# Kernel tuning notes

Hardware: AMD Instinct MI355X
Metric: run time of the kernel (lower is better)

The kernel has to match this reference:

```python
import jax, jax.numpy as jnp
import numpy as np

D_MODEL, D_STATE, D_CONV, EXPAND, L = 512, 16, 4, 2, 2048
D_INNER = EXPAND * D_MODEL


def _dwconv_causal(x, w, b):
    # x: (L, D), w: (D, K), b: (D,). torch Conv1d(groups=D, padding=K-1)[..., :L]
    K = w.shape[1]
    xp = jnp.pad(x, ((K - 1, 0), (0, 0)))
    windows = jnp.stack([xp[k:k + x.shape[0]] for k in range(K)], axis=-1)  # (L, D, K)
    return jnp.einsum('ldk,dk->ld', windows, w) + b


def _ssm_dir(x, inW, inb, cw, cb, xpW, xpb, dtW, dtb, outW, outb, A_log, Dp):
    xz = x @ inW + inb                      # (L, 2*Di)
    x_ssm, z = xz[:, :D_INNER], xz[:, D_INNER:]
    x_ssm = _dwconv_causal(x_ssm, cw, cb)   # (L, Di)
    sp = jax.nn.silu(x_ssm) @ xpW + xpb     # (L, Di + 2*S)
    delta = sp[:, :D_INNER]
    B = sp[:, D_INNER:D_INNER + D_STATE]
    C = sp[:, D_INNER + D_STATE:]
    dt = jax.nn.softplus(delta @ dtW + dtb)  # (L, Di)
    A = -jnp.exp(A_log)                      # (Di, S)
    dA = jnp.exp(dt[:, :, None] * A[None])                      # (L, Di, S)
    dBu = dt[:, :, None] * B[:, None, :] * x_ssm[:, :, None]    # (L, Di, S)

    def step(h, inp):
        a, bu = inp
        h = a * h + bu
        return h, h

    h0 = jnp.zeros((D_INNER, D_STATE), x.dtype)
    _, hs = jax.lax.scan(step, h0, (dA, dBu))   # (L, Di, S)
    y = jnp.einsum('lds,ls->ld', hs, C) + Dp * x_ssm
    return (y * jax.nn.silu(z)) @ outW + outb


def _make_params(key):
    ks = jax.random.split(key, 32)
    i = iter(range(32))
    def w(shape, scale=0.02):
        return (jax.random.normal(ks[next(i)], shape, jnp.float32) * scale)
    p = {}
    for pre in ('fwd_', 'bwd_'):
        p[pre + 'in_W'] = w((D_MODEL, 2 * D_INNER))
        p[pre + 'in_b'] = w((2 * D_INNER,))
        p[pre + 'conv_w'] = w((D_INNER, D_CONV), 0.1)
        p[pre + 'conv_b'] = w((D_INNER,))
        p[pre + 'xp_W'] = w((D_INNER, D_INNER + 2 * D_STATE))
        p[pre + 'xp_b'] = w((D_INNER + 2 * D_STATE,))
        p[pre + 'dt_W'] = w((D_INNER, D_INNER))
        p[pre + 'dt_b'] = w((D_INNER,))
        p[pre + 'out_W'] = w((D_INNER, D_MODEL))
        p[pre + 'out_b'] = w((D_MODEL,))
    p['A_log'] = jax.random.normal(ks[next(i)], (D_INNER, D_STATE), jnp.float32) * 0.5
    p['D_param'] = jnp.ones((D_INNER,), jnp.float32)
    p['fusion_W'] = w((2 * D_MODEL, D_MODEL))
    p['fusion_b'] = w((D_MODEL,))
    return p


def setup_inputs() -> dict:
    key = jax.random.key(0)
    kx, kp = jax.random.split(key)
    inp = {'x': jax.random.normal(kx, (L, D_MODEL), jnp.float32)}
    inp.update(_make_params(kp))
    return inp


def reference(x,
              fwd_in_W, fwd_in_b, fwd_conv_w, fwd_conv_b, fwd_xp_W, fwd_xp_b,
              fwd_dt_W, fwd_dt_b, fwd_out_W, fwd_out_b,
              bwd_in_W, bwd_in_b, bwd_conv_w, bwd_conv_b, bwd_xp_W, bwd_xp_b,
              bwd_dt_W, bwd_dt_b, bwd_out_W, bwd_out_b,
              A_log, D_param, fusion_W, fusion_b):
    out_fwd = _ssm_dir(x, fwd_in_W, fwd_in_b, fwd_conv_w, fwd_conv_b,
                       fwd_xp_W, fwd_xp_b, fwd_dt_W, fwd_dt_b,
                       fwd_out_W, fwd_out_b, A_log, D_param)
    out_bwd = _ssm_dir(x[::-1], bwd_in_W, bwd_in_b, bwd_conv_w, bwd_conv_b,
                       bwd_xp_W, bwd_xp_b, bwd_dt_W, bwd_dt_b,
                       bwd_out_W, bwd_out_b, A_log, D_param)[::-1]
    return jnp.concatenate([out_fwd, out_bwd], axis=-1) @ fusion_W + fusion_b
```

## Files before the change

kernel.cpp:

```cpp
#include <hip/hip_runtime.h>
#include <cmath>

#define L_SEQ 2048
#define DM 512
#define DI 1024
#define DS 16
#define NSP 1056
#define NC 64
#define CL 32

typedef unsigned short ushortT;
typedef unsigned int u32;
typedef __attribute__((ext_vector_type(8))) short short8;
typedef __attribute__((ext_vector_type(4))) float float4_t;
typedef __attribute__((address_space(1))) u32 gu32;
typedef __attribute__((address_space(3))) u32 lu32;

__device__ __forceinline__ float sigm(float x) { return 1.0f / (1.0f + __expf(-x)); }

__device__ __forceinline__ ushortT f2bf(float f) {
    unsigned u = __float_as_uint(f);
    unsigned r = u + 0x7FFFu + ((u >> 16) & 1u);
    return (ushortT)(r >> 16);
}
__device__ __forceinline__ float b2f(ushortT u) {
    return __uint_as_float(((u32)u) << 16);
}

__device__ __forceinline__ void gl2lds16(const ushortT* g, ushortT* l) {
    __builtin_amdgcn_global_load_lds((gu32*)g, (lu32*)l, 16, 0, 0);
}

struct WC {
    const float* src[11];
    ushortT* dst[11];
    int ss[11], soff[11], ds_[11], tN[11], mode[11];
    int off[12];
};

__global__ __launch_bounds__(256) void prep_all(
    WC wc, int nW,
    const float* __restrict__ x, ushortT* __restrict__ xb,
    const float* __restrict__ xpb0, const float* __restrict__ xpb1,
    const float* __restrict__ dtW0, const float* __restrict__ dtW1,
    const float* __restrict__ dtb0, const float* __restrict__ dtb1,
    const float* __restrict__ outb0, const float* __restrict__ outb1,
    const float* __restrict__ fuW, const float* __restrict__ fub,
    float* __restrict__ BFdt0, float* __restrict__ BFdt1, float* __restrict__ BFof)
{
    __shared__ ushortT t[32][33];
    __shared__ float red[256];
    int b = blockIdx.x;
    int tid = threadIdx.x;
    if (b < nW) {
        int m = 0;
        while (b >= wc.off[m + 1]) ++m;
        int tl = b - wc.off[m];
        int n0 = (tl % wc.tN[m]) * 32;
        int k0 = (tl / wc.tN[m]) * 32;
        const float* W = wc.src[m];
        ushortT* D = wc.dst[m];
        int ss = wc.ss[m], soff = wc.soff[m], ds = wc.ds_[m];
        int tx = tid & 31, ty = tid >> 5;
        if (wc.mode[m] == 1) {
            #pragma unroll
            for (int i = 0; i < 32; i += 8)
                D[(size_t)(k0 + ty + i) * ds + n0 + tx] =
                    f2bf(W[(size_t)(k0 + ty + i) * ss + soff + n0 + tx]);
        } else {
            #pragma unroll
            for (int i = 0; i < 32; i += 8)
                t[ty + i][tx] = f2bf(W[(size_t)(k0 + ty + i) * ss + soff + n0 + tx]);
            __syncthreads();
            #pragma unroll
            for (int i = 0; i < 32; i += 8)
                D[(size_t)(n0 + ty + i) * ds + k0 + tx] = t[tx][ty + i];
        }
        return;
    }
    b -= nW;
    if (b < 1024) {
        int i = (b * 256 + tid) * 4;
        float4_t v = *(const float4_t*)(x + i);
        xb[i + 0] = f2bf(v[0]); xb[i + 1] = f2bf(v[1]);
        xb[i + 2] = f2bf(v[2]); xb[i + 3] = f2bf(v[3]);
        return;
    }
    int o = b - 1024;
    float acc = 0.0f;
    if (o < 2112) {
        int dir = o >= 1056;
        int m = o - dir * 1056;
        const float* xpb = dir ? xpb1 : xpb0;
        float* BF = dir ? BFdt1 : BFdt0;
        if (m >= 1024) {
            if (tid == 0) BF[m] = xpb[m];
            return;
        }
        const float* dtW = dir ? dtW1 : dtW0;
        const float* dtb = dir ? dtb1 : dtb0;
        for (int n = tid; n < 1024; n += 256) acc += xpb[n] * dtW[n * 1024 + m];
        red[tid] = acc;
        __syncthreads();
        for (int s = 128; s > 0; s >>= 1) {
            if (tid < s) red[tid] += red[tid + s];
            __syncthreads();
        }
        if (tid == 0) BF[m] = red[0] + dtb[m];
    } else {
        int n = o - 2112;
        for (int j = tid; j < 1024; j += 256) {
            float ob = (j < 512) ? outb0[j] : outb1[j - 512];
            acc += ob * fuW[(size_t)j * 512 + n];
        }
        red[tid] = acc;
        __syncthreads();
        for (int s = 128; s > 0; s >>= 1) {
            if (tid < s) red[tid] += red[tid + s];
            __syncthreads();
        }
        if (tid == 0) BFof[n] = red[0] + fub[n];
    }
}

template<int BM, int BN>
__device__ __forceinline__ void gemm_core(
    ushortT* As, ushortT* Bs, int bm, int bn,
    const ushortT* __restrict__ A, int lda, int revA,
    const ushortT* __restrict__ A2, int dualK,
    const ushortT* __restrict__ W,
    const float* __restrict__ bias,
    float* __restrict__ Cf, int ldcf,
    float* __restrict__ Cf2, int ldcf2, int Nsplit,
    ushortT* __restrict__ Cb, int ldcb,
    ushortT* __restrict__ Cb2, int ldcb2,
    int M, int N, int K, int epi)
{
    constexpr int BK = 64;
    constexpr int MI = BM / 32;
    constexpr int NI = BN / 32;
    constexpr int CA = BM / 32;
    constexpr int CB = BN / 32;
    constexpr int ABUF = BM * BK;
    constexpr int BBUF = BN * BK;

    const int tid  = threadIdx.x;
    const int wave = tid >> 6;
    const int lane = tid & 63;
    const int quad = lane >> 4;
    const int r    = lane & 15;
    const int wm   = (wave >> 1) * (BM / 2);
    const int wn   = (wave & 1) * (BN / 2);

    const int lrow = lane >> 3;
    const int lk   = ((lane & 7) ^ lrow) * 8;

    const ushortT* gA[CA]; const ushortT* gA2[CA]; ushortT* lA[CA];
    #pragma unroll
    for (int c = 0; c < CA; ++c) {
        int row = bm + c * 32 + wave * 8 + lrow;
        int r0 = revA ? (M - 1 - row) : row;
        gA[c] = A + (size_t)r0 * lda + lk;
        gA2[c] = dualK ? (A2 + (size_t)(M - 1 - row) * lda + lk) : gA[c];
        lA[c] = &As[(c * 32 + wave * 8) * BK];
    }
    const ushortT* gB[CB]; ushortT* lB[CB];
    #pragma unroll
    for (int c = 0; c < CB; ++c) {
        int row = bn + c * 32 + wave * 8 + lrow;
        if (row > N - 1) row = N - 1;
        gB[c] = W + (size_t)row * K + lk;
        lB[c] = &Bs[(c * 32 + wave * 8) * BK];
    }

    float4_t acc[MI][NI];
    #pragma unroll
    for (int i = 0; i < MI; ++i)
        #pragma unroll
        for (int j = 0; j < NI; ++j)
            acc[i][j] = (float4_t){0.f, 0.f, 0.f, 0.f};

    const int nsteps = K >> 6;

    auto stage = [&](int step, int buf) {
        int kq = step << 6;
        #pragma unroll
        for (int c = 0; c < CA; ++c) {
            const ushortT* s = (!dualK || kq < 1024) ? gA[c] + kq : gA2[c] + (kq - 1024);
            gl2lds16(s, lA[c] + buf * ABUF);
        }
        #pragma unroll
        for (int c = 0; c < CB; ++c)
            gl2lds16(gB[c] + kq, lB[c] + buf * BBUF);
    };
    auto compute = [&](int buf) {
        #pragma unroll
        for (int kh = 0; kh < 2; ++kh) {
            const int slot = (((kh * 4 + quad) ^ (lane & 7)) * 8);
            short8 af[MI], bf[NI];
            #pragma unroll
            for (int mi = 0; mi < MI; ++mi)
                af[mi] = *(const short8*)&As[buf * ABUF + (wm + mi * 16 + r) * BK + slot];
            #pragma unroll
            for (int ni = 0; ni < NI; ++ni)
                bf[ni] = *(const short8*)&Bs[buf * BBUF + (wn + ni * 16 + r) * BK + slot];
            #pragma unroll
            for (int mi = 0; mi < MI; ++mi)
                #pragma unroll
                for (int ni = 0; ni < NI; ++ni)
                    acc[mi][ni] = __builtin_amdgcn_mfma_f32_16x16x32_bf16(
                        af[mi], bf[ni], acc[mi][ni], 0, 0, 0);
        }
    };

    stage(0, 0);
    for (int i = 0; i < nsteps; i += 2) {
        __syncthreads();
        if (i + 1 < nsteps) stage(i + 1, 1);
        compute(0);
        __syncthreads();
        if (i + 2 < nsteps) stage(i + 2, 0);
        compute(1);
    }

    #pragma unroll
    for (int mi = 0; mi < MI; ++mi) {
        int rowb = bm + wm + mi * 16 + quad * 4;
        #pragma unroll
        for (int ni = 0; ni < NI; ++ni) {
            int gn = bn + wn + ni * 16 + r;
            if (gn < N) {
                float bv = bias ? bias[gn] : 0.0f;
                #pragma unroll
                for (int j = 0; j < 4; ++j) {
                    int orow = rowb + j;
                    float v = acc[mi][ni][j] + bv;
                    if (gn < Nsplit) {
                        if (epi == 1) v = (v > 20.0f) ? v : log1pf(__expf(v));
                        if (Cf) Cf[(size_t)orow * ldcf + gn] = v;
                        if (Cb) Cb[(size_t)orow * ldcb + gn] = f2bf(v);
                    } else {
                        if (Cf2) Cf2[(size_t)orow * ldcf2 + gn - Nsplit] = v;
                        if (Cb2) Cb2[(size_t)orow * ldcb2 + gn - Nsplit] = f2bf(v);
                    }
                }
            }
        }
    }
}

template<int BM, int BN>
__global__ __launch_bounds__(256) void gemm_bf16(
    const ushortT* __restrict__ A, int lda, long long Astr, int revAmode,
    const ushortT* __restrict__ W, long long Wstr,
    const float* __restrict__ bias0, const float* __restrict__ bias1,
    float* __restrict__ Cf, int ldcf, long long Cfstr,
    float* __restrict__ Cf2, int ldcf2, long long Cf2str, int Nsplit,
    ushortT* __restrict__ Cb, int ldcb, long long Cbstr,
    ushortT* __restrict__ Cb2, int ldcb2, long long Cb2str,
    int swz, int M, int N, int K, int epi)
{
    __shared__ ushortT As[2 * BM * 64];
    __shared__ ushortT Bs[2 * BN * 64];
    int bx = blockIdx.x, by = blockIdx.y, dir = blockIdx.z;
    if (swz) {
        int gx = gridDim.x, gy = gridDim.y, gz = gridDim.z;
        long long b = ((long long)dir * gy + by) * gx + bx;
        int xc = (int)(b & 7);
        long long k = b >> 3;
        if (gz == 2) {
            dir = xc & 1;
            int q = xc >> 1;
            if (swz == 1) { int qc = gx >> 2; bx = q * qc + (int)(k % qc); by = (int)(k / qc); }
            else          { int qc = gy >> 2; by = q * qc + (int)(k % qc); bx = (int)(k / qc); }
        } else {
            if (swz == 1) { int qc = gx >> 3; bx = xc * qc + (int)(k % qc); by = (int)(k / qc); }
            else          { int qc = gy >> 3; by = xc * qc + (int)(k % qc); bx = (int)(k / qc); }
        }
    }
    const ushortT* Ad = A;
    const ushortT* A2 = A;
    int revA = 0, dualK = 0;
    if (revAmode == 3) { dualK = 1; A2 = A + Astr; }
    else { Ad += (size_t)dir * Astr; revA = (revAmode == 2) ? dir : revAmode; }
    gemm_core<BM, BN>(As, Bs, by * BM, bx * BN,
        Ad, lda, revA, A2, dualK,
        W + (size_t)dir * Wstr,
        dir ? bias1 : bias0,
        Cf ? Cf + (size_t)dir * Cfstr : nullptr, ldcf,
        Cf2 ? Cf2 + (size_t)dir * Cf2str : nullptr, ldcf2, Nsplit,
        Cb ? Cb + (size_t)dir * Cbstr : nullptr, ldcb,
        Cb2 ? Cb2 + (size_t)dir * Cb2str : nullptr, ldcb2,
        M, N, K, epi);
}

__global__ __launch_bounds__(256) void gemm_fold(
    const ushortT* __restrict__ WtDt, const ushortT* __restrict__ XpD,
    ushortT* __restrict__ WtXpF,
    const ushortT* __restrict__ WtFu, const ushortT* __restrict__ OutC,
    ushortT* __restrict__ WtOF2)
{
    __shared__ ushortT As[2 * 64 * 64];
    __shared__ ushortT Bs[2 * 64 * 64];
    int z = blockIdx.z;
    if (z < 2) {
        gemm_core<64, 64>(As, Bs, blockIdx.y * 64, blockIdx.x * 64,
            WtDt + (size_t)z * DI * DI, DI, 0, nullptr, 0,
            XpD + (size_t)z * DI * DI,
            nullptr, nullptr, 0, nullptr, 0, DI,
            WtXpF + (size_t)z * NSP * DI, DI, nullptr, 0,
            DI, DI, DI, 0);
    } else {
        if (blockIdx.y >= 8) return;
        int d = z - 2;
        gemm_core<64, 64>(As, Bs, blockIdx.y * 64, blockIdx.x * 64,
            WtFu + (size_t)d * DM, DI, 0, nullptr, 0,
            OutC + (size_t)d * DI * DM,
            nullptr, nullptr, 0, nullptr, 0, DI,
            WtOF2 + (size_t)d * DI, 2 * DI, nullptr, 0,
            DM, DI, DM, 0);
    }
}

__global__ __launch_bounds__(256) void conv_k(
    const ushortT* __restrict__ XSb,
    const float* __restrict__ cw0, const float* __restrict__ cw1,
    const float* __restrict__ cb0, const float* __restrict__ cb1,
    ushortT* __restrict__ SCb)
{
    int dir = blockIdx.z;
    XSb += (size_t)dir * L_SEQ * DI;
    SCb += (size_t)dir * L_SEQ * DI;
    const float* cw = dir ? cw1 : cw0;
    const float* cb = dir ? cb1 : cb0;
    int idx = blockIdx.x * 256 + threadIdx.x;
    int d = idx & (DI - 1);
    int l = idx >> 10;
    float w0 = cw[d * 4 + 0], w1 = cw[d * 4 + 1], w2 = cw[d * 4 + 2], w3 = cw[d * 4 + 3];
    float acc = cb[d];
    if (l >= 3) acc += b2f(XSb[(size_t)(l - 3) * DI + d]) * w0;
    if (l >= 2) acc += b2f(XSb[(size_t)(l - 2) * DI + d]) * w1;
    if (l >= 1) acc += b2f(XSb[(size_t)(l - 1) * DI + d]) * w2;
    acc += b2f(XSb[(size_t)l * DI + d]) * w3;
    SCb[idx] = f2bf(acc * sigm(acc));
}

__global__ __launch_bounds__(256) void scanA_k(
    const ushortT* __restrict__ DTb, const ushortT* __restrict__ XSb,
    const float* __restrict__ BC, const float* __restrict__ Alog,
    const float* __restrict__ cw0, const float* __restrict__ cw1,
    const float* __restrict__ cb0, const float* __restrict__ cb1,
    float* __restrict__ Pend, float* __restrict__ Hl)
{
    __shared__ float Bsh[CL][DS];
    int dir = blockIdx.z;
    int c = blockIdx.y;
    int d = blockIdx.x * 256 + threadIdx.x;
    DTb += (size_t)dir * L_SEQ * DI;
    XSb += (size_t)dir * L_SEQ * DI;
    BC  += (size_t)dir * L_SEQ * 32;
    const float* cw = dir ? cw1 : cw0;
    const float* cb = dir ? cb1 : cb0;
    int l0 = c * CL;
    for (int i = threadIdx.x; i < CL * DS; i += 256) {
        int ll = i >> 4, ss = i & 15;
        Bsh[ll][ss] = BC[(size_t)(l0 + ll) * 32 + ss];
    }
    __syncthreads();
    float w0 = cw[d * 4 + 0], w1 = cw[d * 4 + 1], w2 = cw[d * 4 + 2], w3 = cw[d * 4 + 3];
    float cbv = cb[d];
    float x3 = (l0 >= 3) ? b2f(XSb[(size_t)(l0 - 3) * DI + d]) : 0.f;
    float x2 = (l0 >= 2) ? b2f(XSb[(size_t)(l0 - 2) * DI + d]) : 0.f;
    float x1 = (l0 >= 1) ? b2f(XSb[(size_t)(l0 - 1) * DI + d]) : 0.f;
    float Ae[DS], h[DS], P[DS];
    #pragma unroll
    for (int s = 0; s < DS; ++s) { Ae[s] = -__expf(Alog[d * DS + s]); h[s] = 0.f; P[s] = 1.f; }
    for (int t = 0; t < CL; ++t) {
        int l = l0 + t;
        float x0 = b2f(XSb[(size_t)l * DI + d]);
        float xv = cbv + w0 * x3 + w1 * x2 + w2 * x1 + w3 * x0;
        x3 = x2; x2 = x1; x1 = x0;
        float dt = b2f(DTb[(size_t)l * DI + d]);
        float dtx = dt * xv;
        #pragma unroll
        for (int s = 0; s < DS; ++s) {
            float e = __expf(dt * Ae[s]);
            h[s] = e * h[s] + dtx * Bsh[t][s];
            P[s] *= e;
        }
    }
    size_t o = ((size_t)(dir * NC + c) * DI + d) * DS;
    #pragma unroll
    for (int s = 0; s < DS; ++s) { Pend[o + s] = P[s]; Hl[o + s] = h[s]; }
}

__global__ __launch_bounds__(256) void scanB_k(
    const float* __restrict__ Pend, const float* __restrict__ Hl, float* __restrict__ Hs)
{
    int idx = blockIdx.x * 256 + threadIdx.x;
    float h = 0.f;
    int ds = idx & 16383;
    int dir = idx >> 14;
    for (int c = 0; c < NC; ++c) {
        size_t o = ((size_t)(dir * NC + c)) * (DI * DS) + ds;
        Hs[o] = h;
        h = Pend[o] * h + Hl[o];
    }
}

__global__ __launch_bounds__(256) void scanC_k(
    const ushortT* __restrict__ DTb, const ushortT* __restrict__ XSb,
    const float* __restrict__ BC, const ushortT* __restrict__ Zb,
    const float* __restrict__ Alog, const float* __restrict__ Dp,
    const float* __restrict__ cw0, const float* __restrict__ cw1,
    const float* __restrict__ cb0, const float* __restrict__ cb1,
    const float* __restrict__ Hs, ushortT* __restrict__ Gb)
{
    __shared__ float Bsh[CL][DS];
    __shared__ float Csh[CL][DS];
    int dir = blockIdx.z;
    int c = blockIdx.y;
    int d = blockIdx.x * 256 + threadIdx.x;
    DTb += (size_t)dir * L_SEQ * DI;
    XSb += (size_t)dir * L_SEQ * DI;
    BC  += (size_t)dir * L_SEQ * 32;
    Zb  += (size_t)dir * L_SEQ * DI;
    Gb  += (size_t)dir * L_SEQ * DI;
    const float* cw = dir ? cw1 : cw0;
    const float* cb = dir ? cb1 : cb0;
    int l0 = c * CL;
    for (int i = threadIdx.x; i < CL * DS; i += 256) {
        int ll = i >> 4, ss = i & 15;
        size_t base = (size_t)(l0 + ll) * 32;
        Bsh[ll][ss] = BC[base + ss];
        Csh[ll][ss] = BC[base + DS + ss];
    }
    __syncthreads();
    float w0 = cw[d * 4 + 0], w1 = cw[d * 4 + 1], w2 = cw[d * 4 + 2], w3 = cw[d * 4 + 3];
    float cbv = cb[d];
    float x3 = (l0 >= 3) ? b2f(XSb[(size_t)(l0 - 3) * DI + d]) : 0.f;
    float x2 = (l0 >= 2) ? b2f(XSb[(size_t)(l0 - 2) * DI + d]) : 0.f;
    float x1 = (l0 >= 1) ? b2f(XSb[(size_t)(l0 - 1) * DI + d]) : 0.f;
    float Ae[DS], h[DS];
    size_t o = ((size_t)(dir * NC + c) * DI + d) * DS;
    #pragma unroll
    for (int s = 0; s < DS; ++s) { Ae[s] = -__expf(Alog[d * DS + s]); h[s] = Hs[o + s]; }
    float dpv = Dp[d];
    for (int t = 0; t < CL; ++t) {
        int l = l0 + t;
        float x0 = b2f(XSb[(size_t)l * DI + d]);
        float xv = cbv + w0 * x3 + w1 * x2 + w2 * x1 + w3 * x0;
        x3 = x2; x2 = x1; x1 = x0;
        float dt = b2f(DTb[(size_t)l * DI + d]);
        float dtx = dt * xv;
        float y = 0.f;
        #pragma unroll
        for (int s = 0; s < DS; ++s) {
            float e = __expf(dt * Ae[s]);
            h[s] = e * h[s] + dtx * Bsh[t][s];
            y += h[s] * Csh[t][s];
        }
        y += dpv * xv;
        float z = b2f(Zb[(size_t)l * DI + d]);
        Gb[(size_t)l * DI + d] = f2bf(y * (z * sigm(z)));
    }
}

extern "C" void kernel_launch(void* const* d_in, const int* in_sizes, int n_in,
                              void* d_out, int out_size, void* d_ws, size_t ws_size,
                              hipStream_t stream)
{
    (void)in_sizes; (void)n_in; (void)out_size; (void)ws_size;
    const float* x = (const float*)d_in[0];
    const float* inW[2]  = {(const float*)d_in[1],  (const float*)d_in[11]};
    const float* inb[2]  = {(const float*)d_in[2],  (const float*)d_in[12]};
    const float* cw[2]   = {(const float*)d_in[3],  (const float*)d_in[13]};
    const float* cb[2]   = {(const float*)d_in[4],  (const float*)d_in[14]};
    const float* xpW[2]  = {(const float*)d_in[5],  (const float*)d_in[15]};
    const float* xpb[2]  = {(const float*)d_in[6],  (const float*)d_in[16]};
    const float* dtW[2]  = {(const float*)d_in[7],  (const float*)d_in[17]};
    const float* dtb[2]  = {(const float*)d_in[8],  (const float*)d_in[18]};
    const float* outW[2] = {(const float*)d_in[9],  (const float*)d_in[19]};
    const float* outb[2] = {(const float*)d_in[10], (const float*)d_in[20]};
    const float* Alog = (const float*)d_in[21];
    const float* Dp   = (const float*)d_in[22];
    const float* fuW  = (const float*)d_in[23];
    const float* fub  = (const float*)d_in[24];
    float* out = (float*)d_out;

    float* ws = (float*)d_ws;
    size_t off = 0;
    auto alloc = [&](size_t n) { float* p = ws + off; off += n; return p; };
    float* BCf  = alloc((size_t)2 * L_SEQ * 32);
    float* Pend = alloc((size_t)2 * NC * DI * DS);
    float* Hl   = alloc((size_t)2 * NC * DI * DS);
    float* Hs   = alloc((size_t)2 * NC * DI * DS);
    float* BFdt0 = alloc(1056);
    float* BFdt1 = alloc(1056);
    float* BFof  = alloc(512);

    ushortT* wsu = (ushortT*)(ws + off);
    size_t uoff = 0;
    auto ualloc = [&](size_t n) { ushortT* p = wsu + uoff; uoff += n; return p; };
    ushortT* WtIn  = ualloc((size_t)2 * (2 * DI) * DM);
    ushortT* WtDt  = ualloc((size_t)2 * DI * DI);
    ushortT* WtFu  = ualloc((size_t)DM * DI);
    ushortT* WtXpF = ualloc((size_t)2 * NSP * DI);
    ushortT* XpD   = ualloc((size_t)2 * DI * DI);
    ushortT* OutC  = ualloc((size_t)2 * DI * DM);
    ushortT* WtOF2 = ualloc((size_t)DM * 2 * DI);
    ushortT* XB    = ualloc((size_t)L_SEQ * DM);
    ushortT* XSb   = ualloc((size_t)2 * L_SEQ * DI);
    ushortT* Zb    = ualloc((size_t)2 * L_SEQ * DI);
    ushortT* SCb   = ualloc((size_t)2 * L_SEQ * DI);
    ushortT* DTbB  = ualloc((size_t)2 * L_SEQ * DI);
    ushortT* Gb    = ualloc((size_t)2 * L_SEQ * DI);

    dim3 blk(256);

    WC wc;
    struct E { const float* s; ushortT* d; int ss, so, ds, N, K, mode; };
    E es[11] = {
        {inW[0],  WtIn,                          2 * DI, 0,    DM, 2 * DI, DM, 0},
        {inW[1],  WtIn + (size_t)2 * DI * DM,    2 * DI, 0,    DM, 2 * DI, DM, 0},
        {dtW[0],  WtDt,                          DI,     0,    DI, DI,     DI, 0},
        {dtW[1],  WtDt + (size_t)DI * DI,        DI,     0,    DI, DI,     DI, 0},
        {fuW,     WtFu,                          DM,     0,    DI, DM,     DI, 0},
        {xpW[0],  WtXpF + (size_t)DI * DI,       NSP,    DI,   DI, 32,     DI, 0},
        {xpW[1],  WtXpF + (size_t)NSP * DI + (size_t)DI * DI, NSP, DI, DI, 32, DI, 0},
        {xpW[0],  XpD,                           NSP,    0,    DI, DI,     DI, 1},
        {xpW[1],  XpD + (size_t)DI * DI,         NSP,    0,    DI, DI,     DI, 1},
        {outW[0], OutC,                          DM,     0,    DM, DM,     DI, 1},
        {outW[1], OutC + (size_t)DI * DM,        DM,     0,    DM, DM,     DI, 1},
    };
    wc.off[0] = 0;
    for (int m = 0; m < 11; ++m) {
        wc.src[m] = es[m].s; wc.dst[m] = es[m].d;
        wc.ss[m] = es[m].ss; wc.soff[m] = es[m].so; wc.ds_[m] = es[m].ds;
        wc.tN[m] = es[m].N / 32; wc.mode[m] = es[m].mode;
        wc.off[m + 1] = wc.off[m] + (es[m].N / 32) * (es[m].K / 32);
    }
    int nW = wc.off[11];
    prep_all<<<dim3(nW + 1024 + 2624), blk, 0, stream>>>(
        wc, nW, x, XB,
        xpb[0], xpb[1], dtW[0], dtW[1], dtb[0], dtb[1],
        outb[0], outb[1], fuW, fub, BFdt0, BFdt1, BFof);

    gemm_fold<<<dim3(16, 16, 4), blk, 0, stream>>>(WtDt, XpD, WtXpF, WtFu, OutC, WtOF2);

    gemm_bf16<128, 64><<<dim3(32, 16, 2), blk, 0, stream>>>(
        XB, DM, 0, 2, WtIn, (long long)2 * DI * DM, inb[0], inb[1],
        nullptr, 0, 0, nullptr, 0, 0, DI,
        XSb, DI, (long long)L_SEQ * DI, Zb, DI, (long long)L_SEQ * DI,
        1, L_SEQ, 2 * DI, DM, 0);
    conv_k<<<dim3(L_SEQ * DI / 256, 1, 2), blk, 0, stream>>>(
        XSb, cw[0], cw[1], cb[0], cb[1], SCb);
    gemm_bf16<128, 64><<<dim3((NSP + 63) / 64, 16, 2), blk, 0, stream>>>(
        SCb, DI, (long long)L_SEQ * DI, 0, WtXpF, (long long)NSP * DI, BFdt0, BFdt1,
        nullptr, 0, 0, BCf, 32, (long long)L_SEQ * 32, DI,
        DTbB, DI, (long long)L_SEQ * DI, nullptr, 0, 0,
        2, L_SEQ, NSP, DI, 1);
    scanA_k<<<dim3(DI / 256, NC, 2), blk, 0, stream>>>(
        DTbB, XSb, BCf, Alog, cw[0], cw[1], cb[0], cb[1], Pend, Hl);
    scanB_k<<<dim3(2 * DI * DS / 256), blk, 0, stream>>>(Pend, Hl, Hs);
    scanC_k<<<dim3(DI / 256, NC, 2), blk, 0, stream>>>(
        DTbB, XSb, BCf, Zb, Alog, Dp, cw[0], cw[1], cb[0], cb[1], Hs, Gb);
    gemm_bf16<64, 64><<<dim3(DM / 64, 32, 1), blk, 0, stream>>>(
        Gb, DI, (long long)L_SEQ * DI, 3, WtOF2, 0, BFof, BFof,
        out, DM, 0, nullptr, 0, 0, DM,
        nullptr, 0, 0, nullptr, 0, 0,
        2, L_SEQ, DM, 2 * DI, 0);
}
```

Measured before the change: 326.3 us.

## Merge fold and in-projection GEMMs into one launch, vectorize conv, retile output GEMM

Merges the weight-folding GEMMs and the input-projection GEMM into a single mega kernel dispatched by blockIdx.z, so one launch replaces two and the independent work can overlap. The depthwise conv kernel now handles four channels per thread using 8-byte vector loads and stores. The final fused output GEMM moves from a 64x64 to a 64x32 tile, doubling the block count to fill more CUs. The mega kernel sizes LDS for the 128x64 tile in every block, which may lower occupancy for the smaller-tile branches, and many of its blocks exit immediately.

```diff
diff --git a/kernel.cpp b/kernel.cpp
--- a/kernel.cpp
+++ b/kernel.cpp
@@ -12,6 +12,7 @@
 typedef unsigned short ushortT;
 typedef unsigned int u32;
 typedef __attribute__((ext_vector_type(8))) short short8;
+typedef __attribute__((ext_vector_type(4))) unsigned short ushort4_t;
 typedef __attribute__((ext_vector_type(4))) float float4_t;
 typedef __attribute__((address_space(1))) u32 gu32;
 typedef __attribute__((address_space(3))) u32 lu32;
@@ -249,6 +250,55 @@
     }
 }
 
+__global__ __launch_bounds__(256) void mega_k(
+    const ushortT* __restrict__ XB, const ushortT* __restrict__ WtIn,
+    const float* __restrict__ inb0, const float* __restrict__ inb1,
+    ushortT* __restrict__ XSb, ushortT* __restrict__ Zb,
+    const ushortT* __restrict__ WtDt, const ushortT* __restrict__ XpD,
+    ushortT* __restrict__ WtXpF,
+    const ushortT* __restrict__ WtFu, const ushortT* __restrict__ OutC,
+    ushortT* __restrict__ WtOF2)
+{
+    __shared__ ushortT As[2 * 128 * 64];
+    __shared__ ushortT Bs[2 * 64 * 64];
+    int z = blockIdx.z;
+    if (z < 2) {
+        long long b = ((long long)z * 16 + blockIdx.y) * 32 + blockIdx.x;
+        int xc = (int)(b & 7);
+        long long k = b >> 3;
+        int dir = xc & 1;
+        int q = xc >> 1;
+        int bx = q * 8 + (int)(k % 8);
+        int by = (int)(k / 8);
+        gemm_core<128, 64>(As, Bs, by * 128, bx * 64,
+            XB, DM, dir, nullptr, 0,
+            WtIn + (size_t)dir * 2 * DI * DM,
+            dir ? inb1 : inb0,
+            nullptr, 0, nullptr, 0, DI,
+            XSb + (size_t)dir * L_SEQ * DI, DI,
+            Zb + (size_t)dir * L_SEQ * DI, DI,
+            L_SEQ, 2 * DI, DM, 0);
+    } else if (z < 4) {
+        if (blockIdx.x >= 16) return;
+        int d = z - 2;
+        gemm_core<64, 64>(As, Bs, blockIdx.y * 64, blockIdx.x * 64,
+            WtDt + (size_t)d * DI * DI, DI, 0, nullptr, 0,
+            XpD + (size_t)d * DI * DI,
+            nullptr, nullptr, 0, nullptr, 0, DI,
+            WtXpF + (size_t)d * NSP * DI, DI, nullptr, 0,
+            DI, DI, DI, 0);
+    } else {
+        if (blockIdx.x >= 16 || blockIdx.y >= 8) return;
+        int d = z - 4;
+        gemm_core<64, 64>(As, Bs, blockIdx.y * 64, blockIdx.x * 64,
+            WtFu + (size_t)d * DM, DI, 0, nullptr, 0,
+            OutC + (size_t)d * DI * DM,
+            nullptr, nullptr, 0, nullptr, 0, DI,
+            WtOF2 + (size_t)d * DI, 2 * DI, nullptr, 0,
+            DM, DI, DM, 0);
+    }
+}
+
 template<int BM, int BN>
 __global__ __launch_bounds__(256) void gemm_bf16(
     const ushortT* __restrict__ A, int lda, long long Astr, int revAmode,
@@ -294,34 +344,6 @@
         M, N, K, epi);
 }
 
-__global__ __launch_bounds__(256) void gemm_fold(
-    const ushortT* __restrict__ WtDt, const ushortT* __restrict__ XpD,
-    ushortT* __restrict__ WtXpF,
-    const ushortT* __restrict__ WtFu, const ushortT* __restrict__ OutC,
-    ushortT* __restrict__ WtOF2)
-{
-    __shared__ ushortT As[2 * 64 * 64];
-    __shared__ ushortT Bs[2 * 64 * 64];
-    int z = blockIdx.z;
-    if (z < 2) {
-        gemm_core<64, 64>(As, Bs, blockIdx.y * 64, blockIdx.x * 64,
-            WtDt + (size_t)z * DI * DI, DI, 0, nullptr, 0,
-            XpD + (size_t)z * DI * DI,
-            nullptr, nullptr, 0, nullptr, 0, DI,
-            WtXpF + (size_t)z * NSP * DI, DI, nullptr, 0,
-            DI, DI, DI, 0);
-    } else {
-        if (blockIdx.y >= 8) return;
-        int d = z - 2;
-        gemm_core<64, 64>(As, Bs, blockIdx.y * 64, blockIdx.x * 64,
-            WtFu + (size_t)d * DM, DI, 0, nullptr, 0,
-            OutC + (size_t)d * DI * DM,
-            nullptr, nullptr, 0, nullptr, 0, DI,
-            WtOF2 + (size_t)d * DI, 2 * DI, nullptr, 0,
-            DM, DI, DM, 0);
-    }
-}
-
 __global__ __launch_bounds__(256) void conv_k(
     const ushortT* __restrict__ XSb,
     const float* __restrict__ cw0, const float* __restrict__ cw1,
@@ -333,16 +355,22 @@
     SCb += (size_t)dir * L_SEQ * DI;
     const float* cw = dir ? cw1 : cw0;
     const float* cb = dir ? cb1 : cb0;
-    int idx = blockIdx.x * 256 + threadIdx.x;
-    int d = idx & (DI - 1);
+    int idx = (blockIdx.x * 256 + threadIdx.x) * 4;
+    int d4 = idx & (DI - 1);
     int l = idx >> 10;
-    float w0 = cw[d * 4 + 0], w1 = cw[d * 4 + 1], w2 = cw[d * 4 + 2], w3 = cw[d * 4 + 3];
-    float acc = cb[d];
-    if (l >= 3) acc += b2f(XSb[(size_t)(l - 3) * DI + d]) * w0;
-    if (l >= 2) acc += b2f(XSb[(size_t)(l - 2) * DI + d]) * w1;
-    if (l >= 1) acc += b2f(XSb[(size_t)(l - 1) * DI + d]) * w2;
-    acc += b2f(XSb[(size_t)l * DI + d]) * w3;
-    SCb[idx] = f2bf(acc * sigm(acc));
+    ushort4_t r0 = *(const ushort4_t*)(XSb + (size_t)l * DI + d4);
+    ushort4_t r1 = (l >= 1) ? *(const ushort4_t*)(XSb + (size_t)(l - 1) * DI + d4) : (ushort4_t){0,0,0,0};
+    ushort4_t r2 = (l >= 2) ? *(const ushort4_t*)(XSb + (size_t)(l - 2) * DI + d4) : (ushort4_t){0,0,0,0};
+    ushort4_t r3 = (l >= 3) ? *(const ushort4_t*)(XSb + (size_t)(l - 3) * DI + d4) : (ushort4_t){0,0,0,0};
+    ushort4_t outv;
+    #pragma unroll
+    for (int j = 0; j < 4; ++j) {
+        int d = d4 + j;
+        float acc = cb[d] + cw[d * 4 + 0] * b2f(r3[j]) + cw[d * 4 + 1] * b2f(r2[j])
+                  + cw[d * 4 + 2] * b2f(r1[j]) + cw[d * 4 + 3] * b2f(r0[j]);
+        outv[j] = f2bf(acc * sigm(acc));
+    }
+    *(ushort4_t*)(SCb + idx) = outv;
 }
 
 __global__ __launch_bounds__(256) void scanA_k(
@@ -546,14 +574,11 @@
         xpb[0], xpb[1], dtW[0], dtW[1], dtb[0], dtb[1],
         outb[0], outb[1], fuW, fub, BFdt0, BFdt1, BFof);
 
-    gemm_fold<<<dim3(16, 16, 4), blk, 0, stream>>>(WtDt, XpD, WtXpF, WtFu, OutC, WtOF2);
-
-    gemm_bf16<128, 64><<<dim3(32, 16, 2), blk, 0, stream>>>(
-        XB, DM, 0, 2, WtIn, (long long)2 * DI * DM, inb[0], inb[1],
-        nullptr, 0, 0, nullptr, 0, 0, DI,
-        XSb, DI, (long long)L_SEQ * DI, Zb, DI, (long long)L_SEQ * DI,
-        1, L_SEQ, 2 * DI, DM, 0);
-    conv_k<<<dim3(L_SEQ * DI / 256, 1, 2), blk, 0, stream>>>(
+    mega_k<<<dim3(32, 16, 6), blk, 0, stream>>>(
+        XB, WtIn, inb[0], inb[1], XSb, Zb,
+        WtDt, XpD, WtXpF, WtFu, OutC, WtOF2);
+
+    conv_k<<<dim3(L_SEQ * DI / 1024, 1, 2), blk, 0, stream>>>(
         XSb, cw[0], cw[1], cb[0], cb[1], SCb);
     gemm_bf16<128, 64><<<dim3((NSP + 63) / 64, 16, 2), blk, 0, stream>>>(
         SCb, DI, (long long)L_SEQ * DI, 0, WtXpF, (long long)NSP * DI, BFdt0, BFdt1,
@@ -565,7 +590,7 @@
     scanB_k<<<dim3(2 * DI * DS / 256), blk, 0, stream>>>(Pend, Hl, Hs);
     scanC_k<<<dim3(DI / 256, NC, 2), blk, 0, stream>>>(
         DTbB, XSb, BCf, Zb, Alog, Dp, cw[0], cw[1], cb[0], cb[1], Hs, Gb);
-    gemm_bf16<64, 64><<<dim3(DM / 64, 32, 1), blk, 0, stream>>>(
+    gemm_bf16<64, 32><<<dim3(DM / 32, 32, 1), blk, 0, stream>>>(
         Gb, DI, (long long)L_SEQ * DI, 3, WtOF2, 0, BFof, BFof,
         out, DM, 0, nullptr, 0, 0, DM,
         nullptr, 0, 0, nullptr, 0, 0,
```

Measured after the change: 318.2 us. -2.5%, faster.
